# Kernel tuning notes

Measured on AMD Instinct MI355X. Metric: run time of the kernel, lower is better.

## Reference

```python
import jax, jax.numpy as jnp
import numpy as np

EMB = 512
LIN = 64
ATT = 64
H = 8
EPS = 1e-6


def layer_norm(x, eps=EPS):
    # layer norm over last dim, no affine params (matches F.layer_norm w/o weight/bias)
    mu = jnp.mean(x, axis=-1, keepdims=True)
    var = jnp.var(x, axis=-1, keepdims=True)
    return (x - mu) * jax.lax.rsqrt(var + eps)


def setup_inputs() -> dict:
    key = jax.random.key(0)
    k1, k2, k3, k4, k5 = jax.random.split(key, 5)
    B, N = 8, 2048
    x = jax.random.normal(k1, (B, N, EMB), dtype=jnp.float32)
    rel_pos_bias = jax.random.normal(k2, (H, N, N), dtype=jnp.float32)
    invalid_attn_mask = jnp.ones((B, N, N), dtype=jnp.float32)
    uvqk = jax.random.normal(k3, (EMB, LIN * 2 * H + ATT * H * 2), dtype=jnp.float32) * 0.02
    o_w = jax.random.normal(k4, (EMB, LIN * H), dtype=jnp.float32) * (1.0 / np.sqrt(LIN * H))
    o_b = jnp.zeros((EMB,), dtype=jnp.float32)
    return {"x": x, "rel_pos_bias": rel_pos_bias, "invalid_attn_mask": invalid_attn_mask,
            "uvqk": uvqk, "o_w": o_w, "o_b": o_b}


def reference(x, rel_pos_bias, invalid_attn_mask, uvqk, o_w, o_b):
    B, N, D = x.shape
    residual = x
    normed = layer_norm(x)                                   # [B,N,D]
    proj = jax.nn.silu(jnp.einsum('bnd,de->bne', normed, uvqk))  # [B,N,2*LIN*H+2*ATT*H]
    lh = LIN * H
    ah = ATT * H
    u = proj[..., :lh]                                        # [B,N,LIN*H]
    v = proj[..., lh:2 * lh].reshape(B, N, H, LIN)            # [B,N,H,LIN]
    q = proj[..., 2 * lh:2 * lh + ah].reshape(B, N, H, ATT)
    k = proj[..., 2 * lh + ah:].reshape(B, N, H, ATT)
    qk = jnp.einsum('bnhd,bmhd->bhnm', q, k) + rel_pos_bias[None]  # [B,H,N,N]
    qk = jax.nn.silu(qk) * invalid_attn_mask[:, None]
    attn = jnp.einsum('bhnm,bmhd->bnhd', qk, v).reshape(B, N, lh)
    gated = u * layer_norm(attn)
    out = jnp.einsum('bnf,ef->bne', gated, o_w) + o_b          # dropout off (eval)
    return residual + out
```

## Files before the change

### kernel.cpp

```cpp
#include <hip/hip_runtime.h>
#include <stdint.h>

typedef short bf16x8   __attribute__((ext_vector_type(8)));
typedef short short4v  __attribute__((ext_vector_type(4)));
typedef short short8v  __attribute__((ext_vector_type(8)));
typedef float f32x4    __attribute__((ext_vector_type(4)));

typedef __attribute__((address_space(3))) uint32_t lds_u32;
typedef const __attribute__((address_space(1))) uint32_t glob_u32;

__device__ __forceinline__ void gl_lds16(const void* g, void* l) {
  __builtin_amdgcn_global_load_lds((glob_u32*)g, (lds_u32*)l, 16, 0, 0);
}

__device__ __forceinline__ float bf2f(short u) {
  union { float f; uint32_t i; } v; v.i = ((uint32_t)(uint16_t)u) << 16; return v.f;
}
__device__ __forceinline__ short f2bf(float f) {
  union { float f; uint32_t i; } v; v.f = f;
  uint32_t r = v.i + 0x7FFFu + ((v.i >> 16) & 1u);
  return (short)(r >> 16);
}
__device__ __forceinline__ float siluf(float x) {
  return x * __builtin_amdgcn_rcpf(1.0f + __expf(-x));
}
__device__ __forceinline__ f32x4 mfma16(bf16x8 a, bf16x8 b, f32x4 c) {
  return __builtin_amdgcn_mfma_f32_16x16x32_bf16(a, b, c, 0, 0, 0);
}

__global__ __launch_bounds__(256) void k_ln(const float* __restrict__ x, short* __restrict__ xn) {
  int row = blockIdx.x * 4 + (threadIdx.x >> 6);
  int lane = threadIdx.x & 63;
  const float4* xr = (const float4*)(x + (size_t)row * 512);
  float4 a = xr[lane * 2], b = xr[lane * 2 + 1];
  float s  = a.x + a.y + a.z + a.w + b.x + b.y + b.z + b.w;
  float s2 = a.x*a.x + a.y*a.y + a.z*a.z + a.w*a.w + b.x*b.x + b.y*b.y + b.z*b.z + b.w*b.w;
#pragma unroll
  for (int m = 1; m < 64; m <<= 1) { s += __shfl_xor(s, m); s2 += __shfl_xor(s2, m); }
  float mu = s * (1.f / 512.f);
  float rstd = rsqrtf(s2 * (1.f / 512.f) - mu * mu + 1e-6f);
  float v[8] = {a.x, a.y, a.z, a.w, b.x, b.y, b.z, b.w};
  short8v o;
#pragma unroll
  for (int j = 0; j < 8; ++j) o[j] = f2bf((v[j] - mu) * rstd);
  *(short8v*)&xn[(size_t)row * 512 + lane * 8] = o;
}

__global__ __launch_bounds__(256) void k_prep_w(const float* __restrict__ uvqk, short* __restrict__ Wt) {
  __shared__ float t[64][65];
  int k0 = blockIdx.x * 64;
  int c0 = blockIdx.y * 64;
  for (int i = threadIdx.x; i < 64 * 64; i += 256) {
    int r = i >> 6, c = i & 63;
    t[r][c] = uvqk[(size_t)(k0 + r) * 2048 + c0 + c];
  }
  __syncthreads();
  for (int i = threadIdx.x; i < 64 * 64; i += 256) {
    int c = i >> 6, k = i & 63;
    Wt[(size_t)(c0 + c) * 512 + k0 + k] = f2bf(t[k][c]);
  }
}

__global__ __launch_bounds__(256) void k_cast_ow(const float* __restrict__ ow, short* __restrict__ owt) {
  int i = blockIdx.x * 256 + threadIdx.x;
  owt[i] = f2bf(ow[i]);
}

__device__ __forceinline__ void gemm_core(const short* __restrict__ A, const short* __restrict__ Bt,
                                          int t0, int c0, short* As, short* Bs, f32x4 (&acc)[4][4]) {
  int tid = threadIdx.x;
  int w = tid >> 6, lane = tid & 63, l16 = lane & 15, lq = lane >> 4;
  int wm = (w >> 1) * 64, wn = (w & 1) * 64;
  int srow = tid >> 3;
  int sch = (tid & 7) ^ (srow & 7);
  const short* ag = A  + (size_t)(t0 + srow) * 512 + sch * 8;
  const short* bg = Bt + (size_t)(c0 + srow) * 512 + sch * 8;

  for (int k0 = 0; k0 < 512; k0 += 64) {
#pragma unroll
    for (int j = 0; j < 4; ++j) {
      gl_lds16(ag + (size_t)j * 32 * 512 + k0, (char*)As + j * 4096 + w * 1024);
      gl_lds16(bg + (size_t)j * 32 * 512 + k0, (char*)Bs + j * 4096 + w * 1024);
    }
    asm volatile("s_waitcnt vmcnt(0)" ::: "memory");
    __syncthreads();
#pragma unroll
    for (int kk = 0; kk < 2; ++kk) {
      bf16x8 af[4], bf[4];
#pragma unroll
      for (int mi = 0; mi < 4; ++mi) {
        int row = wm + mi * 16 + l16;
        af[mi] = *(const bf16x8*)&As[row * 64 + (((kk * 4 + lq) ^ (l16 & 7)) * 8)];
      }
#pragma unroll
      for (int ni = 0; ni < 4; ++ni) {
        int row = wn + ni * 16 + l16;
        bf[ni] = *(const bf16x8*)&Bs[row * 64 + (((kk * 4 + lq) ^ (l16 & 7)) * 8)];
      }
#pragma unroll
      for (int mi = 0; mi < 4; ++mi)
#pragma unroll
        for (int ni = 0; ni < 4; ++ni)
          acc[mi][ni] = mfma16(af[mi], bf[ni], acc[mi][ni]);
    }
    __syncthreads();
  }
}

__global__ __launch_bounds__(256) void k_gemm1(const short* __restrict__ A, const short* __restrict__ Bt,
                                               short* __restrict__ proj, short* __restrict__ Vt) {
  __shared__ short As[128 * 64], Bs[128 * 64];
  int c0 = blockIdx.x * 128, t0 = blockIdx.y * 128;
  f32x4 acc[4][4] = {};
  gemm_core(A, Bt, t0, c0, As, Bs, acc);
  int tid = threadIdx.x, w = tid >> 6, lane = tid & 63, l16 = lane & 15, lq = lane >> 4;
  int wm = (w >> 1) * 64, wn = (w & 1) * 64;
  bool isv = (c0 >= 512 && c0 < 1024);
#pragma unroll
  for (int mi = 0; mi < 4; ++mi)
#pragma unroll
    for (int ni = 0; ni < 4; ++ni) {
      int c = c0 + wn + ni * 16 + l16;
      int trow = t0 + wm + mi * 16 + lq * 4;
      if (isv) {
        int hh = (c - 512) >> 6, d = (c - 512) & 63;
        int bb = trow >> 11, nn = trow & 2047;
        short4v pv;
#pragma unroll
        for (int i = 0; i < 4; ++i) pv[i] = f2bf(siluf(acc[mi][ni][i]));
        *(short4v*)&Vt[((size_t)(bb * 8 + hh) * 64 + d) * 2048 + nn] = pv;
      } else {
#pragma unroll
        for (int i = 0; i < 4; ++i)
          proj[(size_t)(trow + i) * 2048 + c] = f2bf(siluf(acc[mi][ni][i]));
      }
    }
}

__global__ __launch_bounds__(256, 3) void k_attn(const short* __restrict__ proj,
                                                 const short* __restrict__ Vt,
                                                 const float* __restrict__ rpb,
                                                 const float* __restrict__ maskp,
                                                 float* __restrict__ attn) {
  __shared__ __align__(16) short Ks[2][64 * 64];
  __shared__ __align__(16) short Vs[2][64 * 64];
  __shared__ __align__(16) short Ps[128 * 64];

  int p = blockIdx.x;
  int L = (p & 7) * 128 + (p >> 3);
  int qt = L >> 6, h = (L >> 3) & 7, b = L & 7;
  int n0 = qt * 128;

  int tid = threadIdx.x;
  int w = tid >> 6, lane = tid & 63, l16 = lane & 15, lq = lane >> 4;

  bf16x8 qf[2][2];
#pragma unroll
  for (int mi = 0; mi < 2; ++mi)
#pragma unroll
    for (int kk = 0; kk < 2; ++kk) {
      int n = n0 + w * 32 + mi * 16 + l16;
      qf[mi][kk] = *(const bf16x8*)&proj[(size_t)(b * 2048 + n) * 2048 + 1024 + h * 64 + kk * 32 + lq * 8];
    }

  int j8 = lane >> 3, c8 = lane & 7;
  int srcc = (c8 ^ j8) * 8;
  const short* kg = proj + (size_t)(b * 2048) * 2048 + 1536 + h * 64 + srcc;
  const short* vg = Vt + (size_t)((b * 8 + h) * 64) * 2048 + srcc;

  const float* rp_t = rpb   + (size_t)h * 4194304 + (size_t)(n0 + w * 32 + lq * 4) * 2048 + l16;
  const float* mk_t = maskp + (size_t)b * 4194304 + (size_t)(n0 + w * 32 + lq * 4) * 2048 + l16;

  f32x4 acc_o[2][4] = {};

#pragma unroll
  for (int j = 0; j < 2; ++j) {
    gl_lds16(kg + (size_t)(w * 16 + j * 8 + j8) * 2048, &Ks[0][w * 1024 + j * 512]);
    gl_lds16(vg + (size_t)(w * 16 + j * 8 + j8) * 2048, &Vs[0][w * 1024 + j * 512]);
  }
  asm volatile("s_waitcnt vmcnt(0)" ::: "memory");
  __builtin_amdgcn_s_barrier();

  for (int t = 0; t < 32; ++t) {
    int kv0 = t << 6;
    const short* Kc = Ks[t & 1];
    const short* Vc = Vs[t & 1];
    short* Kn = Ks[(t & 1) ^ 1];
    short* Vn = Vs[(t & 1) ^ 1];
    int kvn = (kv0 + 64) & 2047;

#pragma unroll
    for (int j = 0; j < 2; ++j) {
      gl_lds16(kg + (size_t)(kvn + w * 16 + j * 8 + j8) * 2048, &Kn[w * 1024 + j * 512]);
      gl_lds16(vg + (size_t)(w * 16 + j * 8 + j8) * 2048 + kvn, &Vn[w * 1024 + j * 512]);
    }

    const float* rp_i = rp_t + kv0;
    const float* mk_i = mk_t + kv0;
    float rv0[4][4], mv0[4][4];
#pragma unroll
    for (int ni = 0; ni < 4; ++ni)
#pragma unroll
      for (int i = 0; i < 4; ++i) {
        rv0[ni][i] = rp_i[(size_t)i * 2048 + ni * 16];
        mv0[ni][i] = mk_i[(size_t)i * 2048 + ni * 16];
      }

    f32x4 s[2][4] = {};
#pragma unroll
    for (int kk = 0; kk < 2; ++kk) {
      bf16x8 kf[4];
#pragma unroll
      for (int ni = 0; ni < 4; ++ni)
        kf[ni] = *(const bf16x8*)&Kc[(ni * 16 + l16) * 64 + (((kk * 4 + lq) ^ (l16 & 7)) * 8)];
#pragma unroll
      for (int mi = 0; mi < 2; ++mi)
#pragma unroll
        for (int ni = 0; ni < 4; ++ni)
          s[mi][ni] = mfma16(qf[mi][kk], kf[ni], s[mi][ni]);
    }

    float rv1[4][4], mv1[4][4];
#pragma unroll
    for (int ni = 0; ni < 4; ++ni)
#pragma unroll
      for (int i = 0; i < 4; ++i) {
        rv1[ni][i] = rp_i[(size_t)(16 + i) * 2048 + ni * 16];
        mv1[ni][i] = mk_i[(size_t)(16 + i) * 2048 + ni * 16];
      }

#pragma unroll
    for (int ni = 0; ni < 4; ++ni)
#pragma unroll
      for (int i = 0; i < 4; ++i) {
        float xx = s[0][ni][i] + rv0[ni][i];
        float pv = siluf(xx) * mv0[ni][i];
        int row = w * 32 + lq * 4 + i;
        int cb = ni * 2 + (l16 >> 3);
        *(short*)((char*)Ps + row * 128 + (((cb ^ (row & 7)) << 4) + (l16 & 7) * 2)) = f2bf(pv);
      }
#pragma unroll
    for (int ni = 0; ni < 4; ++ni)
#pragma unroll
      for (int i = 0; i < 4; ++i) {
        float xx = s[1][ni][i] + rv1[ni][i];
        float pv = siluf(xx) * mv1[ni][i];
        int row = w * 32 + 16 + lq * 4 + i;
        int cb = ni * 2 + (l16 >> 3);
        *(short*)((char*)Ps + row * 128 + (((cb ^ (row & 7)) << 4) + (l16 & 7) * 2)) = f2bf(pv);
      }

#pragma unroll
    for (int ks = 0; ks < 2; ++ks) {
      bf16x8 pf[2], vf[4];
#pragma unroll
      for (int mi = 0; mi < 2; ++mi) {
        int rp = w * 32 + mi * 16 + l16;
        pf[mi] = *(const bf16x8*)((const char*)Ps + rp * 128 + (((ks * 4 + lq) ^ (rp & 7)) * 16));
      }
#pragma unroll
      for (int ni = 0; ni < 4; ++ni)
        vf[ni] = *(const bf16x8*)&Vc[(ni * 16 + l16) * 64 + (((ks * 4 + lq) ^ (l16 & 7)) * 8)];
#pragma unroll
      for (int mi = 0; mi < 2; ++mi)
#pragma unroll
        for (int ni = 0; ni < 4; ++ni)
          acc_o[mi][ni] = mfma16(pf[mi], vf[ni], acc_o[mi][ni]);
    }

    asm volatile("s_waitcnt vmcnt(0)" ::: "memory");
    __builtin_amdgcn_s_barrier();
  }

#pragma unroll
  for (int mi = 0; mi < 2; ++mi)
#pragma unroll
    for (int ni = 0; ni < 4; ++ni)
#pragma unroll
      for (int i = 0; i < 4; ++i) {
        int n = n0 + w * 32 + mi * 16 + lq * 4 + i;
        attn[(size_t)(b * 2048 + n) * 512 + h * 64 + ni * 16 + l16] = acc_o[mi][ni][i];
      }
}

__global__ __launch_bounds__(256) void k_gate(const float* __restrict__ attn, const short* __restrict__ proj,
                                              short* __restrict__ gated) {
  int row = blockIdx.x * 4 + (threadIdx.x >> 6);
  int lane = threadIdx.x & 63;
  const float4* ar = (const float4*)(attn + (size_t)row * 512);
  float4 a = ar[lane * 2], b = ar[lane * 2 + 1];
  float s  = a.x + a.y + a.z + a.w + b.x + b.y + b.z + b.w;
  float s2 = a.x*a.x + a.y*a.y + a.z*a.z + a.w*a.w + b.x*b.x + b.y*b.y + b.z*b.z + b.w*b.w;
#pragma unroll
  for (int m = 1; m < 64; m <<= 1) { s += __shfl_xor(s, m); s2 += __shfl_xor(s2, m); }
  float mu = s * (1.f / 512.f);
  float rstd = rsqrtf(s2 * (1.f / 512.f) - mu * mu + 1e-6f);
  float v[8] = {a.x, a.y, a.z, a.w, b.x, b.y, b.z, b.w};
  short8v u = *(const short8v*)&proj[(size_t)row * 2048 + lane * 8];
  short8v g;
#pragma unroll
  for (int j = 0; j < 8; ++j) g[j] = f2bf(bf2f(u[j]) * ((v[j] - mu) * rstd));
  *(short8v*)&gated[(size_t)row * 512 + lane * 8] = g;
}

__global__ __launch_bounds__(256) void k_gemm2(const short* __restrict__ A, const short* __restrict__ Bt,
                                               const float* __restrict__ ob, const float* __restrict__ x,
                                               float* __restrict__ out) {
  __shared__ short As[128 * 64], Bs[128 * 64];
  int c0 = blockIdx.x * 128, t0 = blockIdx.y * 128;
  f32x4 acc[4][4] = {};
  gemm_core(A, Bt, t0, c0, As, Bs, acc);
  int tid = threadIdx.x, w = tid >> 6, lane = tid & 63, l16 = lane & 15, lq = lane >> 4;
  int wm = (w >> 1) * 64, wn = (w & 1) * 64;
#pragma unroll
  for (int mi = 0; mi < 4; ++mi)
#pragma unroll
    for (int ni = 0; ni < 4; ++ni) {
      int e = c0 + wn + ni * 16 + l16;
      float bias = ob[e];
#pragma unroll
      for (int i = 0; i < 4; ++i) {
        int t = t0 + wm + mi * 16 + lq * 4 + i;
        out[(size_t)t * 512 + e] = acc[mi][ni][i] + bias + x[(size_t)t * 512 + e];
      }
    }
}

extern "C" void kernel_launch(void* const* d_in, const int* in_sizes, int n_in,
                              void* d_out, int out_size, void* d_ws, size_t ws_size,
                              hipStream_t stream) {
  const float* x    = (const float*)d_in[0];
  const float* rpb  = (const float*)d_in[1];
  const float* mask = (const float*)d_in[2];
  const float* uvqk = (const float*)d_in[3];
  const float* o_w  = (const float*)d_in[4];
  const float* o_b  = (const float*)d_in[5];
  float* out = (float*)d_out;

  char* p = (char*)d_ws;
  short* xn   = (short*)p; p += 16384ull * 512 * 2;
  short* Wt   = (short*)p; p += 2048ull * 512 * 2;
  short* owt  = (short*)p; p += 512ull * 512 * 2;
  short* proj = (short*)p; p += 16384ull * 2048 * 2;
  short* Vt   = (short*)p; p += 8ull * 8 * 64 * 2048 * 2;
  float* attn = (float*)p; p += 16384ull * 512 * 4;
  short* gated = xn;

  k_ln    <<<4096, 256, 0, stream>>>(x, xn);
  k_prep_w<<<dim3(8, 32), 256, 0, stream>>>(uvqk, Wt);
  k_cast_ow<<<1024, 256, 0, stream>>>(o_w, owt);
  k_gemm1 <<<dim3(16, 128), 256, 0, stream>>>(xn, Wt, proj, Vt);
  k_attn  <<<1024, 256, 0, stream>>>(proj, Vt, rpb, mask, attn);
  k_gate  <<<4096, 256, 0, stream>>>(attn, proj, gated);
  k_gemm2 <<<dim3(4, 128), 256, 0, stream>>>(gated, owt, o_b, x, out);
}
```

Before: 443.4 us.

## Transpose QK score MFMA so bias/mask loads and P stores vectorize

Swaps the MFMA operand order for the score tile so each lane holds four consecutive key columns of one query row. That lets the rel_pos_bias and mask reads become 16-byte vector loads and the P tile be written to LDS as packed 4-element stores instead of scalar shorts. It also skips the wasted K/V prefetch on the last iteration and raises wave priority around the MFMA blocks. The cost is more complex swizzle indexing that must stay consistent between the P writes and reads.

New measurement: 392.3 us. 11.5% less time.

```diff
diff --git a/kernel.cpp b/kernel.cpp
--- a/kernel.cpp
+++ b/kernel.cpp
@@ -168,8 +168,8 @@
   const short* kg = proj + (size_t)(b * 2048) * 2048 + 1536 + h * 64 + srcc;
   const short* vg = Vt + (size_t)((b * 8 + h) * 64) * 2048 + srcc;
 
-  const float* rp_t = rpb   + (size_t)h * 4194304 + (size_t)(n0 + w * 32 + lq * 4) * 2048 + l16;
-  const float* mk_t = maskp + (size_t)b * 4194304 + (size_t)(n0 + w * 32 + lq * 4) * 2048 + l16;
+  const float* rp_t = rpb   + (size_t)h * 4194304 + (size_t)(n0 + w * 32 + l16) * 2048 + lq * 4;
+  const float* mk_t = maskp + (size_t)b * 4194304 + (size_t)(n0 + w * 32 + l16) * 2048 + lq * 4;
 
   f32x4 acc_o[2][4] = {};
 
@@ -185,28 +185,31 @@
     int kv0 = t << 6;
     const short* Kc = Ks[t & 1];
     const short* Vc = Vs[t & 1];
-    short* Kn = Ks[(t & 1) ^ 1];
-    short* Vn = Vs[(t & 1) ^ 1];
-    int kvn = (kv0 + 64) & 2047;
-
-#pragma unroll
-    for (int j = 0; j < 2; ++j) {
-      gl_lds16(kg + (size_t)(kvn + w * 16 + j * 8 + j8) * 2048, &Kn[w * 1024 + j * 512]);
-      gl_lds16(vg + (size_t)(w * 16 + j * 8 + j8) * 2048 + kvn, &Vn[w * 1024 + j * 512]);
-    }
-
-    const float* rp_i = rp_t + kv0;
-    const float* mk_i = mk_t + kv0;
-    float rv0[4][4], mv0[4][4];
+
+    if (t < 31) {
+      short* Kn = Ks[(t & 1) ^ 1];
+      short* Vn = Vs[(t & 1) ^ 1];
+      int kvn = kv0 + 64;
+#pragma unroll
+      for (int j = 0; j < 2; ++j) {
+        gl_lds16(kg + (size_t)(kvn + w * 16 + j * 8 + j8) * 2048, &Kn[w * 1024 + j * 512]);
+        gl_lds16(vg + (size_t)(w * 16 + j * 8 + j8) * 2048 + kvn, &Vn[w * 1024 + j * 512]);
+      }
+    }
+
+    f32x4 rv0[4], mv0[4];
+#pragma unroll
+    for (int ni = 0; ni < 4; ++ni) {
+      rv0[ni] = *(const f32x4*)(rp_t + kv0 + ni * 16);
+      mv0[ni] = *(const f32x4*)(mk_t + kv0 + ni * 16);
+    }
+
+    f32x4 s[4][2];
 #pragma unroll
     for (int ni = 0; ni < 4; ++ni)
 #pragma unroll
-      for (int i = 0; i < 4; ++i) {
-        rv0[ni][i] = rp_i[(size_t)i * 2048 + ni * 16];
-        mv0[ni][i] = mk_i[(size_t)i * 2048 + ni * 16];
-      }
-
-    f32x4 s[2][4] = {};
+      for (int mi = 0; mi < 2; ++mi) s[ni][mi] = (f32x4){0.f, 0.f, 0.f, 0.f};
+    __builtin_amdgcn_s_setprio(1);
 #pragma unroll
     for (int kk = 0; kk < 2; ++kk) {
       bf16x8 kf[4];
@@ -214,49 +217,59 @@
       for (int ni = 0; ni < 4; ++ni)
         kf[ni] = *(const bf16x8*)&Kc[(ni * 16 + l16) * 64 + (((kk * 4 + lq) ^ (l16 & 7)) * 8)];
 #pragma unroll
-      for (int mi = 0; mi < 2; ++mi)
-#pragma unroll
-        for (int ni = 0; ni < 4; ++ni)
-          s[mi][ni] = mfma16(qf[mi][kk], kf[ni], s[mi][ni]);
-    }
-
-    float rv1[4][4], mv1[4][4];
-#pragma unroll
-    for (int ni = 0; ni < 4; ++ni)
-#pragma unroll
-      for (int i = 0; i < 4; ++i) {
-        rv1[ni][i] = rp_i[(size_t)(16 + i) * 2048 + ni * 16];
-        mv1[ni][i] = mk_i[(size_t)(16 + i) * 2048 + ni * 16];
-      }
-
-#pragma unroll
-    for (int ni = 0; ni < 4; ++ni)
-#pragma unroll
-      for (int i = 0; i < 4; ++i) {
-        float xx = s[0][ni][i] + rv0[ni][i];
-        float pv = siluf(xx) * mv0[ni][i];
-        int row = w * 32 + lq * 4 + i;
-        int cb = ni * 2 + (l16 >> 3);
-        *(short*)((char*)Ps + row * 128 + (((cb ^ (row & 7)) << 4) + (l16 & 7) * 2)) = f2bf(pv);
-      }
-#pragma unroll
-    for (int ni = 0; ni < 4; ++ni)
-#pragma unroll
-      for (int i = 0; i < 4; ++i) {
-        float xx = s[1][ni][i] + rv1[ni][i];
-        float pv = siluf(xx) * mv1[ni][i];
-        int row = w * 32 + 16 + lq * 4 + i;
-        int cb = ni * 2 + (l16 >> 3);
-        *(short*)((char*)Ps + row * 128 + (((cb ^ (row & 7)) << 4) + (l16 & 7) * 2)) = f2bf(pv);
-      }
-
+      for (int ni = 0; ni < 4; ++ni)
+#pragma unroll
+        for (int mi = 0; mi < 2; ++mi)
+          s[ni][mi] = mfma16(kf[ni], qf[mi][kk], s[ni][mi]);
+    }
+    __builtin_amdgcn_s_setprio(0);
+
+    f32x4 rv1[4], mv1[4];
+#pragma unroll
+    for (int ni = 0; ni < 4; ++ni) {
+      rv1[ni] = *(const f32x4*)(rp_t + 16 * 2048 + kv0 + ni * 16);
+      mv1[ni] = *(const f32x4*)(mk_t + 16 * 2048 + kv0 + ni * 16);
+    }
+
+    {
+      int row = w * 32 + l16;
+      char* pr = (char*)Ps + row * 128;
+      int swz = (l16 & 7) << 4;
+#pragma unroll
+      for (int ni = 0; ni < 4; ++ni) {
+        short4v pk;
+#pragma unroll
+        for (int i = 0; i < 4; ++i) {
+          float xx = s[ni][0][i] + rv0[ni][i];
+          pk[i] = f2bf(siluf(xx) * mv0[ni][i]);
+        }
+        *(short4v*)(pr + ((ni * 32 + lq * 8) ^ swz)) = pk;
+      }
+    }
+    {
+      int row = w * 32 + 16 + l16;
+      char* pr = (char*)Ps + row * 128;
+      int swz = (l16 & 7) << 4;
+#pragma unroll
+      for (int ni = 0; ni < 4; ++ni) {
+        short4v pk;
+#pragma unroll
+        for (int i = 0; i < 4; ++i) {
+          float xx = s[ni][1][i] + rv1[ni][i];
+          pk[i] = f2bf(siluf(xx) * mv1[ni][i]);
+        }
+        *(short4v*)(pr + ((ni * 32 + lq * 8) ^ swz)) = pk;
+      }
+    }
+
+    __builtin_amdgcn_s_setprio(1);
 #pragma unroll
     for (int ks = 0; ks < 2; ++ks) {
       bf16x8 pf[2], vf[4];
 #pragma unroll
       for (int mi = 0; mi < 2; ++mi) {
         int rp = w * 32 + mi * 16 + l16;
-        pf[mi] = *(const bf16x8*)((const char*)Ps + rp * 128 + (((ks * 4 + lq) ^ (rp & 7)) * 16));
+        pf[mi] = *(const bf16x8*)((const char*)Ps + rp * 128 + (((ks * 4 + lq) << 4) ^ ((l16 & 7) << 4)));
       }
 #pragma unroll
       for (int ni = 0; ni < 4; ++ni)
@@ -267,6 +280,7 @@
         for (int ni = 0; ni < 4; ++ni)
           acc_o[mi][ni] = mfma16(pf[mi], vf[ni], acc_o[mi][ni]);
     }
+    __builtin_amdgcn_s_setprio(0);
 
     asm volatile("s_waitcnt vmcnt(0)" ::: "memory");
     __builtin_amdgcn_s_barrier();
```
